# Kernel optimization log

Measured on AMD Instinct MI355X. Metric: run time of the kernel, lower is better.

The kernel has to match this reference:

```python
import jax, jax.numpy as jnp
import numpy as np

INPUT, HIDDEN, OUT = 784, 64, 10
N_TEST = 10000
WVEC = INPUT * HIDDEN + HIDDEN + HIDDEN * OUT + OUT  # 50890
B = 64


def setup_inputs() -> dict:
    key = jax.random.key(0)
    k1, k2, k3, k4, k5 = jax.random.split(key, 5)
    inp1 = jax.random.normal(k1, (B, WVEC), dtype=jnp.float32)
    tar1 = jax.random.normal(k2, (B, WVEC), dtype=jnp.float32)
    inp2 = jax.random.normal(k3, (B, WVEC), dtype=jnp.float32)
    tar2 = jax.random.randint(k4, (B, N_TEST), 0, OUT, dtype=jnp.int64)
    images = jax.random.uniform(k5, (N_TEST, INPUT), dtype=jnp.float32)
    return {"inp1": inp1, "tar1": tar1, "inp2": inp2, "tar2": tar2, "images": images}


def _split_weights(w):
    # w: [B, 50890] -> W1 [B,H,I], B1 [B,H], W2 [B,O,H], B2 [B,O]
    b = w.shape[0]
    o1 = INPUT * HIDDEN
    o2 = o1 + HIDDEN
    o3 = o2 + HIDDEN * OUT
    W1 = w[:, :o1].reshape(b, HIDDEN, INPUT)
    B1 = w[:, o1:o2]
    W2 = w[:, o2:o3].reshape(b, OUT, HIDDEN)
    B2 = w[:, o3:]
    return W1, B1, W2, B2


def reference(inp1, tar1, inp2, tar2, images):
    # loss1: MSE * 20
    loss1 = 20.0 * jnp.mean(jnp.square(inp1 - tar1))
    # loss2: per-sample weight-conditioned MLP over fixed dataset, cross entropy
    W1, B1, W2, B2 = _split_weights(inp2)
    h = jax.nn.relu(jnp.einsum('nd,bhd->bnh', images, W1) + B1[:, None, :])   # [B,N,H]
    logits = jnp.einsum('bnh,boh->bno', h, W2) + B2[:, None, :]               # [B,N,O]
    logp = jax.nn.log_softmax(logits, axis=-1)
    ce = -jnp.take_along_axis(logp, tar2[..., None], axis=-1).squeeze(-1)     # [B,N]
    loss2 = jnp.mean(ce)  # mean over images per sample, then mean over batch
    combined = loss1 + loss2
    return (combined, loss1, loss2)
```

## Files before the change

kernel.cpp:

```cpp
#include <hip/hip_runtime.h>
#include <hip/hip_bf16.h>
#include <stdint.h>

#define INPUT_D 784
#define HIDDEN  64
#define OUTC    10
#define NTEST   10000
#define WVEC    50890
#define NBATCH  64
#define O1      50176
#define O2      50240
#define O3      50880
#define KPAD8   896
#define MPAD    10240
#define MTILES  80
#define NCOLS   4096
#define KTILES  7
#define H2      136
#define SCALE1  0x7F7F7F7Fu
#define CAST_ROWS (MPAD + NCOLS)
#define CAST_GROUPS (CAST_ROWS * (KPAD8/4))

typedef __attribute__((ext_vector_type(8))) short  short8;
typedef __attribute__((ext_vector_type(4))) float  floatx4;
typedef __attribute__((ext_vector_type(4))) int    int4v;
typedef __attribute__((ext_vector_type(8))) int    int8v;

__device__ inline void async_copy16(const void* g, void* lds) {
  __builtin_amdgcn_global_load_lds(
      (const __attribute__((address_space(1))) void*)g,
      (__attribute__((address_space(3))) void*)lds, 16, 0, 0);
}

__global__ void prep_kernel(const float* __restrict__ img, const float* __restrict__ inp2,
                            const float* __restrict__ l1a, const float* __restrict__ l1b,
                            uint8_t* __restrict__ outI, uint8_t* __restrict__ outW,
                            float* __restrict__ accum) {
  const int gtid = blockIdx.x * blockDim.x + threadIdx.x;
  const int nthr = gridDim.x * blockDim.x;
  for (int i = gtid; i < CAST_GROUPS; i += nthr) {
    const int row = i / 224;
    const int c   = (i - row * 224) * 4;
    const float* src;
    uint8_t* dst;
    bool valid;
    if (row < MPAD) {
      valid = (row < NTEST);
      src = img + (size_t)row * INPUT_D;
      dst = outI + (size_t)row * KPAD8;
    } else {
      const int rr = row - MPAD;
      valid = true;
      src = inp2 + (size_t)(rr >> 6) * WVEC + (rr & 63) * INPUT_D;
      dst = outW + (size_t)rr * KPAD8;
    }
    float4 v = make_float4(0.f, 0.f, 0.f, 0.f);
    if (valid && (c + 4) <= INPUT_D) v = *(const float4*)(src + c);
    uint32_t w = 0;
    w = __builtin_amdgcn_cvt_pk_fp8_f32(v.x, v.y, w, false);
    w = __builtin_amdgcn_cvt_pk_fp8_f32(v.z, v.w, w, true);
    *(uint32_t*)(dst + c) = w;
  }
  const int n4 = (NBATCH * WVEC) / 4;
  const float4* A4 = (const float4*)l1a;
  const float4* B4 = (const float4*)l1b;
  float s = 0.f;
  for (int i = gtid; i < n4; i += nthr) {
    float4 x = A4[i], y = B4[i];
    float d0 = x.x - y.x, d1 = x.y - y.y, d2 = x.z - y.z, d3 = x.w - y.w;
    s += d0 * d0 + d1 * d1 + d2 * d2 + d3 * d3;
  }
  for (int off = 32; off; off >>= 1) s += __shfl_down(s, off);
  __shared__ float r[4];
  if ((threadIdx.x & 63) == 0) r[threadIdx.x >> 6] = s;
  __syncthreads();
  if (threadIdx.x == 0) atomicAdd(accum, r[0] + r[1] + r[2] + r[3]);
}

__global__ __launch_bounds__(256)
void gemm_fused(const uint8_t* __restrict__ A,
                const uint8_t* __restrict__ Bm,
                const float* __restrict__ inp2,
                const int* __restrict__ tar2,
                float* __restrict__ accums) {
  __shared__ __align__(16) char smem[65536];
  uint8_t* Abuf[2] = {(uint8_t*)smem,           (uint8_t*)(smem + 32768)};
  uint8_t* Bbuf[2] = {(uint8_t*)(smem + 16384), (uint8_t*)(smem + 49152)};
  __hip_bfloat16* hlds  = (__hip_bfloat16*)smem;
  __hip_bfloat16* w2lds = (__hip_bfloat16*)(smem + 34816);
  float*          B2s   = (float*)(smem + 38912);
  int*            tars  = (int*)(smem + 38992);
  float*          red   = (float*)(smem + 40016);

  const int tid  = threadIdx.x;
  const int lane = tid & 63;
  const int wave = tid >> 6;
  const int wr   = (wave >> 1) * 64;
  const int wc   = (wave & 1) * 64;
  const int row0 = blockIdx.x * 128;
  const int col0 = blockIdx.y * 128;
  const int bbase = col0 >> 6;

  floatx4 acc[4][4];
#pragma unroll
  for (int i = 0; i < 4; ++i)
#pragma unroll
    for (int j = 0; j < 4; ++j) acc[i][j] = (floatx4){0.f, 0.f, 0.f, 0.f};

  const int lr   = lane >> 3;
  const int lcB  = (((lane & 7) ^ lr) * 16);
  const int sxor = lane & 7;
  const int q    = lane >> 4;
  const int c0   = (2 * q) ^ sxor;
  const int c1   = c0 ^ 1;

  const uint8_t* Ag = A  + (size_t)(row0 + wave * 32 + lr) * KPAD8 + lcB;
  const uint8_t* Bg = Bm + (size_t)(col0 + wave * 32 + lr) * KPAD8 + lcB;

#pragma unroll
  for (int c = 0; c < 4; ++c) {
    async_copy16(Ag + (size_t)(c * 8) * KPAD8, Abuf[0] + (wave * 4 + c) * 1024);
    async_copy16(Bg + (size_t)(c * 8) * KPAD8, Bbuf[0] + (wave * 4 + c) * 1024);
  }

#pragma unroll
  for (int kt = 0; kt < KTILES; ++kt) {
    __syncthreads();
    if (kt + 1 < KTILES) {
      const int k0 = (kt + 1) * 128;
#pragma unroll
      for (int c = 0; c < 4; ++c) {
        async_copy16(Ag + (size_t)(c * 8) * KPAD8 + k0, Abuf[(kt + 1) & 1] + (wave * 4 + c) * 1024);
        async_copy16(Bg + (size_t)(c * 8) * KPAD8 + k0, Bbuf[(kt + 1) & 1] + (wave * 4 + c) * 1024);
      }
    }
    const uint8_t* Asrc = Abuf[kt & 1];
    const uint8_t* Bsrc = Bbuf[kt & 1];
    int8v b8[4];
#pragma unroll
    for (int ni = 0; ni < 4; ++ni) {
      const uint8_t* base = Bsrc + (wc + ni * 16 + (lane & 15)) * 128;
      int4v lo = *(const int4v*)(base + c0 * 16);
      int4v hi = *(const int4v*)(base + c1 * 16);
      b8[ni] = (int8v){lo.x, lo.y, lo.z, lo.w, hi.x, hi.y, hi.z, hi.w};
    }
#pragma unroll
    for (int mi = 0; mi < 4; ++mi) {
      const uint8_t* base = Asrc + (wr + mi * 16 + (lane & 15)) * 128;
      int4v lo = *(const int4v*)(base + c0 * 16);
      int4v hi = *(const int4v*)(base + c1 * 16);
      int8v a8 = (int8v){lo.x, lo.y, lo.z, lo.w, hi.x, hi.y, hi.z, hi.w};
#pragma unroll
      for (int ni = 0; ni < 4; ++ni)
        acc[mi][ni] = __builtin_amdgcn_mfma_scale_f32_16x16x128_f8f6f4(
            a8, b8[ni], acc[mi][ni], 0 , 0 ,
            0, SCALE1, 0, SCALE1);
    }
  }
  __syncthreads();

  for (int i = tid; i < 2048; i += 256) {
    const int bi = i >> 10, rem = i & 1023;
    const int o = rem >> 6, k = rem & 63;
    float v = (o < OUTC) ? inp2[(size_t)(bbase + bi) * WVEC + O2 + o * HIDDEN + k] : 0.f;
    w2lds[i] = __float2bfloat16(v);
  }
  if (tid < 20) B2s[tid] = inp2[(size_t)(bbase + tid / 10) * WVEC + O3 + tid % 10];
  {
    const int bi = tid >> 7, m = tid & 127;
    const int sample = row0 + m;
    tars[tid] = (sample < NTEST) ? tar2[(size_t)(bbase + bi) * NTEST + sample] : 0;
  }
#pragma unroll
  for (int ni = 0; ni < 4; ++ni) {
    const int n = wc + ni * 16 + (lane & 15);
    const float b1 = inp2[(size_t)(bbase + (n >> 6)) * WVEC + O1 + (n & 63)];
#pragma unroll
    for (int mi = 0; mi < 4; ++mi) {
      const int m = wr + mi * 16 + q * 4;
#pragma unroll
      for (int r = 0; r < 4; ++r) {
        float v = acc[mi][ni][r] + b1;
        hlds[(size_t)(m + r) * H2 + n] = __float2bfloat16(v > 0.f ? v : 0.f);
      }
    }
  }
  __syncthreads();

  const int col = lane & 15;
  float celocal = 0.f;
#pragma unroll
  for (int i = 0; i < 4; ++i) {
    const int task = wave * 4 + i;
    const int mt = task & 7;
    const int bi = task >> 3;
    short8 af0 = *(const short8*)&hlds[(size_t)(mt * 16 + col) * H2 + bi * 64 + q * 8];
    short8 af1 = *(const short8*)&hlds[(size_t)(mt * 16 + col) * H2 + bi * 64 + 32 + q * 8];
    short8 bf0 = *(const short8*)&w2lds[(bi * 16 + col) * 64 + q * 8];
    short8 bf1 = *(const short8*)&w2lds[(bi * 16 + col) * 64 + 32 + q * 8];
    floatx4 lacc = (floatx4){0.f, 0.f, 0.f, 0.f};
    lacc = __builtin_amdgcn_mfma_f32_16x16x32_bf16(af0, bf0, lacc, 0, 0, 0);
    lacc = __builtin_amdgcn_mfma_f32_16x16x32_bf16(af1, bf1, lacc, 0, 0, 0);
    const float b2 = (col < OUTC) ? B2s[bi * OUTC + col] : 0.f;
#pragma unroll
    for (int r = 0; r < 4; ++r) {
      float lv = (col < OUTC) ? (lacc[r] + b2) : -1e30f;
      float mx = lv;
      mx = fmaxf(mx, __shfl_xor(mx, 1));
      mx = fmaxf(mx, __shfl_xor(mx, 2));
      mx = fmaxf(mx, __shfl_xor(mx, 4));
      mx = fmaxf(mx, __shfl_xor(mx, 8));
      float ex = __expf(lv - mx);
      float sm = ex;
      sm += __shfl_xor(sm, 1);
      sm += __shfl_xor(sm, 2);
      sm += __shfl_xor(sm, 4);
      sm += __shfl_xor(sm, 8);
      const float lse = mx + __logf(sm);
      const int row = mt * 16 + q * 4 + r;
      const int tar = tars[bi * 128 + row];
      if (col == tar && (row0 + row) < NTEST) celocal += (lse - lv);
    }
  }
  for (int off = 32; off; off >>= 1) celocal += __shfl_down(celocal, off);
  if (lane == 0) red[wave] = celocal;
  __syncthreads();
  if (tid == 0) atomicAdd(&accums[1], red[0] + red[1] + red[2] + red[3]);
}

__global__ void finalize(const float* __restrict__ accums, float* __restrict__ out) {
  const float l1 = 20.f * accums[0] / (float)(NBATCH * WVEC);
  const float l2 = accums[1] / (float)(NBATCH * NTEST);
  out[0] = l1 + l2;
  out[1] = l1;
  out[2] = l2;
}

__global__ void loss1_fb(const float* __restrict__ a, const float* __restrict__ b,
                         float* __restrict__ accum) {
  const int n4 = (NBATCH * WVEC) / 4;
  const float4* A4 = (const float4*)a;
  const float4* B4 = (const float4*)b;
  float s = 0.f;
  for (int i = blockIdx.x * blockDim.x + threadIdx.x; i < n4; i += gridDim.x * blockDim.x) {
    float4 x = A4[i], y = B4[i];
    float d0 = x.x - y.x, d1 = x.y - y.y, d2 = x.z - y.z, d3 = x.w - y.w;
    s += d0 * d0 + d1 * d1 + d2 * d2 + d3 * d3;
  }
  for (int off = 32; off; off >>= 1) s += __shfl_down(s, off);
  __shared__ float r[4];
  if ((threadIdx.x & 63) == 0) r[threadIdx.x >> 6] = s;
  __syncthreads();
  if (threadIdx.x == 0) atomicAdd(accum, r[0] + r[1] + r[2] + r[3]);
}

__global__ void naive_ce(const float* __restrict__ inp2, const int* __restrict__ tar2,
                         const float* __restrict__ images, float* __restrict__ accum) {
  const int id = blockIdx.x * blockDim.x + threadIdx.x;
  float ce = 0.f;
  if (id < NBATCH * NTEST) {
    const int b = id / NTEST, n = id % NTEST;
    const float* w = inp2 + (size_t)b * WVEC;
    const float* im = images + (size_t)n * INPUT_D;
    float h[HIDDEN];
    for (int hh = 0; hh < HIDDEN; ++hh) {
      float s = w[O1 + hh];
      for (int d = 0; d < INPUT_D; ++d) s = fmaf(im[d], w[hh * INPUT_D + d], s);
      h[hh] = s > 0.f ? s : 0.f;
    }
    float mx = -1e30f, lg[OUTC];
    for (int o = 0; o < OUTC; ++o) {
      float s = w[O3 + o];
      for (int hh = 0; hh < HIDDEN; ++hh) s = fmaf(h[hh], w[O2 + o * HIDDEN + hh], s);
      lg[o] = s;
      mx = fmaxf(mx, s);
    }
    float sm = 0.f;
    for (int o = 0; o < OUTC; ++o) sm += __expf(lg[o] - mx);
    const float lse = mx + __logf(sm);
    const int t = tar2[(size_t)b * NTEST + n];
    float lt = lg[0];
    for (int o = 1; o < OUTC; ++o) lt = (o == t) ? lg[o] : lt;
    ce = lse - lt;
  }
  for (int off = 32; off; off >>= 1) ce += __shfl_down(ce, off);
  __shared__ float r[4];
  if ((threadIdx.x & 63) == 0) r[threadIdx.x >> 6] = ce;
  __syncthreads();
  if (threadIdx.x == 0) atomicAdd(accum, r[0] + r[1] + r[2] + r[3]);
}

extern "C" void kernel_launch(void* const* d_in, const int* in_sizes, int n_in,
                              void* d_out, int out_size, void* d_ws, size_t ws_size,
                              hipStream_t stream) {
  const float* inp1   = (const float*)d_in[0];
  const float* tar1   = (const float*)d_in[1];
  const float* inp2   = (const float*)d_in[2];
  const int*   tar2   = (const int*)d_in[3];
  const float* images = (const float*)d_in[4];
  float*       out    = (float*)d_out;

  const size_t img_bytes  = (size_t)MPAD * KPAD8;
  const size_t wall_bytes = (size_t)NCOLS * KPAD8;
  const size_t needed     = 256 + img_bytes + wall_bytes;

  if (ws_size >= needed) {
    float* accums = (float*)d_ws;
    uint8_t* imgb = (uint8_t*)d_ws + 256;
    uint8_t* wall = (uint8_t*)d_ws + 256 + img_bytes;
    hipMemsetAsync(d_ws, 0, 256, stream);
    prep_kernel<<<1024, 256, 0, stream>>>(images, inp2, inp1, tar1, imgb, wall, accums);
    gemm_fused<<<dim3(MTILES, 32), 256, 0, stream>>>(imgb, wall, inp2, tar2, accums);
    finalize<<<1, 1, 0, stream>>>(accums, out);
  } else {
    hipMemsetAsync(d_out, 0, 3 * sizeof(float), stream);
    loss1_fb<<<1024, 256, 0, stream>>>(inp1, tar1, out + 1);
    naive_ce<<<(NBATCH * NTEST + 255) / 256, 256, 0, stream>>>(inp2, tar2, images, out + 2);
    finalize<<<1, 1, 0, stream>>>(out + 1, out);
  }
}
```

Before: 194.5 us.

## Use 256-row GEMM tiles, single-buffer LDS, fold finalize into last block

Each GEMM block now covers two 128-row image tiles that share one loaded weight tile, which halves B-operand loads and the grid size. Double-buffered LDS prefetch is replaced by a single-buffer load-sync-compute loop with a launch bound of three blocks per CU. The memset and finalize launches are removed: prep writes per-block loss1 partials and zeroes the counters, and the last GEMM block, found through an atomic counter, reduces them and writes the outputs. The price is lost load/compute overlap, doubled accumulator registers, and reliance on prep's zeroing finishing before the GEMM kernel starts.

```diff
diff --git a/kernel.cpp b/kernel.cpp
--- a/kernel.cpp
+++ b/kernel.cpp
@@ -13,13 +13,15 @@
 #define O3      50880
 #define KPAD8   896
 #define MPAD    10240
-#define MTILES  80
+#define RPAIRS  40
+#define NBLK    (RPAIRS * 32)
 #define NCOLS   4096
 #define KTILES  7
 #define H2      136
 #define SCALE1  0x7F7F7F7Fu
 #define CAST_ROWS (MPAD + NCOLS)
 #define CAST_GROUPS (CAST_ROWS * (KPAD8/4))
+#define PREP_BLOCKS 1024
 
 typedef __attribute__((ext_vector_type(8))) short  short8;
 typedef __attribute__((ext_vector_type(4))) float  floatx4;
@@ -35,7 +37,7 @@
 __global__ void prep_kernel(const float* __restrict__ img, const float* __restrict__ inp2,
                             const float* __restrict__ l1a, const float* __restrict__ l1b,
                             uint8_t* __restrict__ outI, uint8_t* __restrict__ outW,
-                            float* __restrict__ accum) {
+                            float* __restrict__ accums) {
   const int gtid = blockIdx.x * blockDim.x + threadIdx.x;
   const int nthr = gridDim.x * blockDim.x;
   for (int i = gtid; i < CAST_GROUPS; i += nthr) {
@@ -74,38 +76,49 @@
   __shared__ float r[4];
   if ((threadIdx.x & 63) == 0) r[threadIdx.x >> 6] = s;
   __syncthreads();
-  if (threadIdx.x == 0) atomicAdd(accum, r[0] + r[1] + r[2] + r[3]);
-}
-
-__global__ __launch_bounds__(256)
+  if (threadIdx.x == 0) {
+    accums[2 + blockIdx.x] = r[0] + r[1] + r[2] + r[3];
+    if (blockIdx.x == 0) {
+      *(unsigned int*)&accums[0] = 0u;
+      accums[1] = 0.f;
+    }
+  }
+}
+
+__global__ __launch_bounds__(256, 3)
 void gemm_fused(const uint8_t* __restrict__ A,
                 const uint8_t* __restrict__ Bm,
                 const float* __restrict__ inp2,
                 const int* __restrict__ tar2,
-                float* __restrict__ accums) {
-  __shared__ __align__(16) char smem[65536];
-  uint8_t* Abuf[2] = {(uint8_t*)smem,           (uint8_t*)(smem + 32768)};
-  uint8_t* Bbuf[2] = {(uint8_t*)(smem + 16384), (uint8_t*)(smem + 49152)};
+                float* __restrict__ accums,
+                float* __restrict__ out) {
+  __shared__ __align__(16) char smem[49184];
+  uint8_t* Alds0 = (uint8_t*)smem;
+  uint8_t* Alds1 = (uint8_t*)(smem + 16384);
+  uint8_t* Blds  = (uint8_t*)(smem + 32768);
   __hip_bfloat16* hlds  = (__hip_bfloat16*)smem;
   __hip_bfloat16* w2lds = (__hip_bfloat16*)(smem + 34816);
   float*          B2s   = (float*)(smem + 38912);
   int*            tars  = (int*)(smem + 38992);
   float*          red   = (float*)(smem + 40016);
+  int*            flag  = (int*)(smem + 40032);
 
   const int tid  = threadIdx.x;
   const int lane = tid & 63;
   const int wave = tid >> 6;
   const int wr   = (wave >> 1) * 64;
   const int wc   = (wave & 1) * 64;
-  const int row0 = blockIdx.x * 128;
+  const int row0 = blockIdx.x * 256;
   const int col0 = blockIdx.y * 128;
   const int bbase = col0 >> 6;
 
-  floatx4 acc[4][4];
-#pragma unroll
-  for (int i = 0; i < 4; ++i)
-#pragma unroll
-    for (int j = 0; j < 4; ++j) acc[i][j] = (floatx4){0.f, 0.f, 0.f, 0.f};
+  floatx4 acc[2][4][4];
+#pragma unroll
+  for (int t = 0; t < 2; ++t)
+#pragma unroll
+    for (int i = 0; i < 4; ++i)
+#pragma unroll
+      for (int j = 0; j < 4; ++j) acc[t][i][j] = (floatx4){0.f, 0.f, 0.f, 0.f};
 
   const int lr   = lane >> 3;
   const int lcB  = (((lane & 7) ^ lr) * 16);
@@ -117,47 +130,41 @@
   const uint8_t* Ag = A  + (size_t)(row0 + wave * 32 + lr) * KPAD8 + lcB;
   const uint8_t* Bg = Bm + (size_t)(col0 + wave * 32 + lr) * KPAD8 + lcB;
 
-#pragma unroll
-  for (int c = 0; c < 4; ++c) {
-    async_copy16(Ag + (size_t)(c * 8) * KPAD8, Abuf[0] + (wave * 4 + c) * 1024);
-    async_copy16(Bg + (size_t)(c * 8) * KPAD8, Bbuf[0] + (wave * 4 + c) * 1024);
-  }
-
-#pragma unroll
   for (int kt = 0; kt < KTILES; ++kt) {
-    __syncthreads();
-    if (kt + 1 < KTILES) {
-      const int k0 = (kt + 1) * 128;
-#pragma unroll
-      for (int c = 0; c < 4; ++c) {
-        async_copy16(Ag + (size_t)(c * 8) * KPAD8 + k0, Abuf[(kt + 1) & 1] + (wave * 4 + c) * 1024);
-        async_copy16(Bg + (size_t)(c * 8) * KPAD8 + k0, Bbuf[(kt + 1) & 1] + (wave * 4 + c) * 1024);
-      }
-    }
-    const uint8_t* Asrc = Abuf[kt & 1];
-    const uint8_t* Bsrc = Bbuf[kt & 1];
+    const int k0 = kt * 128;
+#pragma unroll
+    for (int c = 0; c < 4; ++c) {
+      const int ch = wave * 4 + c;
+      async_copy16(Ag + (size_t)(c * 8) * KPAD8 + k0,                 Alds0 + ch * 1024);
+      async_copy16(Ag + (size_t)(128 + c * 8) * KPAD8 + k0,           Alds1 + ch * 1024);
+      async_copy16(Bg + (size_t)(c * 8) * KPAD8 + k0,                 Blds  + ch * 1024);
+    }
+    __syncthreads();
     int8v b8[4];
 #pragma unroll
     for (int ni = 0; ni < 4; ++ni) {
-      const uint8_t* base = Bsrc + (wc + ni * 16 + (lane & 15)) * 128;
+      const uint8_t* base = Blds + (wc + ni * 16 + (lane & 15)) * 128;
       int4v lo = *(const int4v*)(base + c0 * 16);
       int4v hi = *(const int4v*)(base + c1 * 16);
       b8[ni] = (int8v){lo.x, lo.y, lo.z, lo.w, hi.x, hi.y, hi.z, hi.w};
     }
 #pragma unroll
-    for (int mi = 0; mi < 4; ++mi) {
-      const uint8_t* base = Asrc + (wr + mi * 16 + (lane & 15)) * 128;
-      int4v lo = *(const int4v*)(base + c0 * 16);
-      int4v hi = *(const int4v*)(base + c1 * 16);
-      int8v a8 = (int8v){lo.x, lo.y, lo.z, lo.w, hi.x, hi.y, hi.z, hi.w};
-#pragma unroll
-      for (int ni = 0; ni < 4; ++ni)
-        acc[mi][ni] = __builtin_amdgcn_mfma_scale_f32_16x16x128_f8f6f4(
-            a8, b8[ni], acc[mi][ni], 0 , 0 ,
-            0, SCALE1, 0, SCALE1);
-    }
-  }
-  __syncthreads();
+    for (int t = 0; t < 2; ++t) {
+      const uint8_t* Asrc = t ? Alds1 : Alds0;
+#pragma unroll
+      for (int mi = 0; mi < 4; ++mi) {
+        const uint8_t* base = Asrc + (wr + mi * 16 + (lane & 15)) * 128;
+        int4v lo = *(const int4v*)(base + c0 * 16);
+        int4v hi = *(const int4v*)(base + c1 * 16);
+        int8v a8 = (int8v){lo.x, lo.y, lo.z, lo.w, hi.x, hi.y, hi.z, hi.w};
+#pragma unroll
+        for (int ni = 0; ni < 4; ++ni)
+          acc[t][mi][ni] = __builtin_amdgcn_mfma_scale_f32_16x16x128_f8f6f4(
+              a8, b8[ni], acc[t][mi][ni], 0, 0, 0, SCALE1, 0, SCALE1);
+      }
+    }
+    __syncthreads();
+  }
 
   for (int i = tid; i < 2048; i += 256) {
     const int bi = i >> 10, rem = i & 1023;
@@ -166,74 +173,95 @@
     w2lds[i] = __float2bfloat16(v);
   }
   if (tid < 20) B2s[tid] = inp2[(size_t)(bbase + tid / 10) * WVEC + O3 + tid % 10];
-  {
-    const int bi = tid >> 7, m = tid & 127;
-    const int sample = row0 + m;
-    tars[tid] = (sample < NTEST) ? tar2[(size_t)(bbase + bi) * NTEST + sample] : 0;
-  }
+  float b1v[4];
 #pragma unroll
   for (int ni = 0; ni < 4; ++ni) {
     const int n = wc + ni * 16 + (lane & 15);
-    const float b1 = inp2[(size_t)(bbase + (n >> 6)) * WVEC + O1 + (n & 63)];
-#pragma unroll
-    for (int mi = 0; mi < 4; ++mi) {
-      const int m = wr + mi * 16 + q * 4;
-#pragma unroll
-      for (int r = 0; r < 4; ++r) {
-        float v = acc[mi][ni][r] + b1;
-        hlds[(size_t)(m + r) * H2 + n] = __float2bfloat16(v > 0.f ? v : 0.f);
-      }
-    }
-  }
-  __syncthreads();
-
+    b1v[ni] = inp2[(size_t)(bbase + (n >> 6)) * WVEC + O1 + (n & 63)];
+  }
   const int col = lane & 15;
   float celocal = 0.f;
 #pragma unroll
-  for (int i = 0; i < 4; ++i) {
-    const int task = wave * 4 + i;
-    const int mt = task & 7;
-    const int bi = task >> 3;
-    short8 af0 = *(const short8*)&hlds[(size_t)(mt * 16 + col) * H2 + bi * 64 + q * 8];
-    short8 af1 = *(const short8*)&hlds[(size_t)(mt * 16 + col) * H2 + bi * 64 + 32 + q * 8];
-    short8 bf0 = *(const short8*)&w2lds[(bi * 16 + col) * 64 + q * 8];
-    short8 bf1 = *(const short8*)&w2lds[(bi * 16 + col) * 64 + 32 + q * 8];
-    floatx4 lacc = (floatx4){0.f, 0.f, 0.f, 0.f};
-    lacc = __builtin_amdgcn_mfma_f32_16x16x32_bf16(af0, bf0, lacc, 0, 0, 0);
-    lacc = __builtin_amdgcn_mfma_f32_16x16x32_bf16(af1, bf1, lacc, 0, 0, 0);
-    const float b2 = (col < OUTC) ? B2s[bi * OUTC + col] : 0.f;
-#pragma unroll
-    for (int r = 0; r < 4; ++r) {
-      float lv = (col < OUTC) ? (lacc[r] + b2) : -1e30f;
-      float mx = lv;
-      mx = fmaxf(mx, __shfl_xor(mx, 1));
-      mx = fmaxf(mx, __shfl_xor(mx, 2));
-      mx = fmaxf(mx, __shfl_xor(mx, 4));
-      mx = fmaxf(mx, __shfl_xor(mx, 8));
-      float ex = __expf(lv - mx);
-      float sm = ex;
-      sm += __shfl_xor(sm, 1);
-      sm += __shfl_xor(sm, 2);
-      sm += __shfl_xor(sm, 4);
-      sm += __shfl_xor(sm, 8);
-      const float lse = mx + __logf(sm);
-      const int row = mt * 16 + q * 4 + r;
-      const int tar = tars[bi * 128 + row];
-      if (col == tar && (row0 + row) < NTEST) celocal += (lse - lv);
-    }
+  for (int t = 0; t < 2; ++t) {
+    const int row0t = row0 + t * 128;
+    {
+      const int bi = tid >> 7, m = tid & 127;
+      const int sample = row0t + m;
+      tars[tid] = (sample < NTEST) ? tar2[(size_t)(bbase + bi) * NTEST + sample] : 0;
+    }
+#pragma unroll
+    for (int ni = 0; ni < 4; ++ni) {
+      const int n = wc + ni * 16 + col;
+#pragma unroll
+      for (int mi = 0; mi < 4; ++mi) {
+        const int m = wr + mi * 16 + q * 4;
+#pragma unroll
+        for (int r = 0; r < 4; ++r) {
+          float v = acc[t][mi][ni][r] + b1v[ni];
+          hlds[(size_t)(m + r) * H2 + n] = __float2bfloat16(v > 0.f ? v : 0.f);
+        }
+      }
+    }
+    __syncthreads();
+#pragma unroll
+    for (int i = 0; i < 4; ++i) {
+      const int task = wave * 4 + i;
+      const int mt = task & 7;
+      const int bi = task >> 3;
+      short8 af0 = *(const short8*)&hlds[(size_t)(mt * 16 + col) * H2 + bi * 64 + q * 8];
+      short8 af1 = *(const short8*)&hlds[(size_t)(mt * 16 + col) * H2 + bi * 64 + 32 + q * 8];
+      short8 bf0 = *(const short8*)&w2lds[(bi * 16 + col) * 64 + q * 8];
+      short8 bf1 = *(const short8*)&w2lds[(bi * 16 + col) * 64 + 32 + q * 8];
+      floatx4 lacc = (floatx4){0.f, 0.f, 0.f, 0.f};
+      lacc = __builtin_amdgcn_mfma_f32_16x16x32_bf16(af0, bf0, lacc, 0, 0, 0);
+      lacc = __builtin_amdgcn_mfma_f32_16x16x32_bf16(af1, bf1, lacc, 0, 0, 0);
+      const float b2 = (col < OUTC) ? B2s[bi * OUTC + col] : 0.f;
+#pragma unroll
+      for (int r = 0; r < 4; ++r) {
+        float lv = (col < OUTC) ? (lacc[r] + b2) : -1e30f;
+        float mx = lv;
+        mx = fmaxf(mx, __shfl_xor(mx, 1));
+        mx = fmaxf(mx, __shfl_xor(mx, 2));
+        mx = fmaxf(mx, __shfl_xor(mx, 4));
+        mx = fmaxf(mx, __shfl_xor(mx, 8));
+        float ex = __expf(lv - mx);
+        float sm = ex;
+        sm += __shfl_xor(sm, 1);
+        sm += __shfl_xor(sm, 2);
+        sm += __shfl_xor(sm, 4);
+        sm += __shfl_xor(sm, 8);
+        const float lse = mx + __logf(sm);
+        const int row = mt * 16 + q * 4 + r;
+        const int tar = tars[bi * 128 + row];
+        if (col == tar && (row0t + row) < NTEST) celocal += (lse - lv);
+      }
+    }
+    __syncthreads();
   }
   for (int off = 32; off; off >>= 1) celocal += __shfl_down(celocal, off);
   if (lane == 0) red[wave] = celocal;
   __syncthreads();
-  if (tid == 0) atomicAdd(&accums[1], red[0] + red[1] + red[2] + red[3]);
-}
-
-__global__ void finalize(const float* __restrict__ accums, float* __restrict__ out) {
-  const float l1 = 20.f * accums[0] / (float)(NBATCH * WVEC);
-  const float l2 = accums[1] / (float)(NBATCH * NTEST);
-  out[0] = l1 + l2;
-  out[1] = l1;
-  out[2] = l2;
+  if (tid == 0) {
+    atomicAdd(&accums[1], red[0] + red[1] + red[2] + red[3]);
+    __threadfence();
+    unsigned int old = atomicAdd((unsigned int*)&accums[0], 1u);
+    *flag = (old == (unsigned int)(NBLK - 1)) ? 1 : 0;
+  }
+  __syncthreads();
+  if (*flag) {
+    float s = 0.f;
+    for (int i = tid; i < PREP_BLOCKS; i += 256) s += accums[2 + i];
+    for (int off = 32; off; off >>= 1) s += __shfl_down(s, off);
+    if (lane == 0) red[wave] = s;
+    __syncthreads();
+    if (tid == 0) {
+      const float l1 = 20.f * (red[0] + red[1] + red[2] + red[3]) / (float)(NBATCH * WVEC);
+      const float l2 = atomicAdd(&accums[1], 0.f) / (float)(NBATCH * NTEST);
+      out[0] = l1 + l2;
+      out[1] = l1;
+      out[2] = l2;
+    }
+  }
 }
 
 __global__ void loss1_fb(const float* __restrict__ a, const float* __restrict__ b,
@@ -290,6 +318,14 @@
   if (threadIdx.x == 0) atomicAdd(accum, r[0] + r[1] + r[2] + r[3]);
 }
 
+__global__ void finalize_fb(const float* __restrict__ accums, float* __restrict__ out) {
+  const float l1 = 20.f * accums[0] / (float)(NBATCH * WVEC);
+  const float l2 = accums[1] / (float)(NBATCH * NTEST);
+  out[0] = l1 + l2;
+  out[1] = l1;
+  out[2] = l2;
+}
+
 extern "C" void kernel_launch(void* const* d_in, const int* in_sizes, int n_in,
                               void* d_out, int out_size, void* d_ws, size_t ws_size,
                               hipStream_t stream) {
@@ -300,22 +336,21 @@
   const float* images = (const float*)d_in[4];
   float*       out    = (float*)d_out;
 
+  const size_t acc_bytes  = 8192;
   const size_t img_bytes  = (size_t)MPAD * KPAD8;
   const size_t wall_bytes = (size_t)NCOLS * KPAD8;
-  const size_t needed     = 256 + img_bytes + wall_bytes;
+  const size_t needed     = acc_bytes + img_bytes + wall_bytes;
 
   if (ws_size >= needed) {
     float* accums = (float*)d_ws;
-    uint8_t* imgb = (uint8_t*)d_ws + 256;
-    uint8_t* wall = (uint8_t*)d_ws + 256 + img_bytes;
-    hipMemsetAsync(d_ws, 0, 256, stream);
-    prep_kernel<<<1024, 256, 0, stream>>>(images, inp2, inp1, tar1, imgb, wall, accums);
-    gemm_fused<<<dim3(MTILES, 32), 256, 0, stream>>>(imgb, wall, inp2, tar2, accums);
-    finalize<<<1, 1, 0, stream>>>(accums, out);
+    uint8_t* imgb = (uint8_t*)d_ws + acc_bytes;
+    uint8_t* wall = (uint8_t*)d_ws + acc_bytes + img_bytes;
+    prep_kernel<<<PREP_BLOCKS, 256, 0, stream>>>(images, inp2, inp1, tar1, imgb, wall, accums);
+    gemm_fused<<<dim3(RPAIRS, 32), 256, 0, stream>>>(imgb, wall, inp2, tar2, accums, out);
   } else {
     hipMemsetAsync(d_out, 0, 3 * sizeof(float), stream);
     loss1_fb<<<1024, 256, 0, stream>>>(inp1, tar1, out + 1);
     naive_ce<<<(NBATCH * NTEST + 255) / 256, 256, 0, stream>>>(inp2, tar2, images, out + 2);
-    finalize<<<1, 1, 0, stream>>>(out + 1, out);
-  }
-}
+    finalize_fb<<<1, 1, 0, stream>>>(out + 1, out);
+  }
+}
```

New measurement: 274.1 us. 40.9% more time.
